# Kernel tuning notes

Measured on AMD Instinct MI355X. Metric: run time of the kernel, lower is better.

The kernel has to match this reference:

```python
import jax, jax.numpy as jnp
import numpy as np

N_NODES = 50000
N_EDGES = 640000
HID = 128
N_LAYERS = 4
BN_EPS = 1e-5


def _bn(h, gamma, beta):
    # train-mode BatchNorm1d over node axis (biased variance, as torch uses for normalization)
    mu = h.mean(axis=0)
    var = h.var(axis=0)
    return gamma * (h - mu) * jax.lax.rsqrt(var + BN_EPS) + beta


def setup_inputs() -> dict:
    key = jax.random.key(0)
    ks = jax.random.split(key, 8)
    s = 1.0 / np.sqrt(HID)
    x = jax.random.normal(ks[0], (N_NODES, HID), dtype=jnp.float32)
    edge_index = jax.random.randint(ks[1], (2, N_EDGES), 0, N_NODES, dtype=jnp.int64)
    edge_attr = jax.random.normal(ks[2], (N_EDGES, HID), dtype=jnp.float32)
    W1 = jax.random.normal(ks[3], (N_LAYERS, HID, HID), dtype=jnp.float32) * s
    b1 = jnp.zeros((N_LAYERS, HID), jnp.float32)
    g1 = jnp.ones((N_LAYERS, HID), jnp.float32)
    be1 = jnp.zeros((N_LAYERS, HID), jnp.float32)
    W2 = jax.random.normal(ks[4], (N_LAYERS, HID, HID), dtype=jnp.float32) * s
    b2 = jnp.zeros((N_LAYERS, HID), jnp.float32)
    bn_g = jnp.ones((N_LAYERS - 1, HID), jnp.float32)
    bn_b = jnp.zeros((N_LAYERS - 1, HID), jnp.float32)
    return {"x": x, "edge_index": edge_index, "edge_attr": edge_attr,
            "W1": W1, "b1": b1, "g1": g1, "be1": be1,
            "W2": W2, "b2": b2, "bn_g": bn_g, "bn_b": bn_b}


def reference(x, edge_index, edge_attr, W1, b1, g1, be1, W2, b2, bn_g, bn_b):
    src, dst = edge_index[0], edge_index[1]
    n = x.shape[0]
    z = x
    for i in range(N_LAYERS):
        # GINEConv: message = relu(x_j + e_ij), sum-aggregate, eps=0
        msg = jax.nn.relu(z[src] + edge_attr)          # [E, H]
        agg = jax.ops.segment_sum(msg, dst, num_segments=n)  # [N, H]
        h = z + agg
        # conv MLP: Linear -> BatchNorm1d -> ReLU -> Linear
        h = h @ W1[i] + b1[i]
        h = jax.nn.relu(_bn(h, g1[i], be1[i]))
        h = h @ W2[i] + b2[i]
        # encoder activation
        z = jax.nn.relu(h)
        # inter-layer batchnorm (not after last layer)
        if i != N_LAYERS - 1:
            z = _bn(z, bn_g[i], bn_b[i])
    return z
```

## Files before the change

### kernel.cpp

```cpp
#include <hip/hip_runtime.h>
#include <hip/hip_bf16.h>

#define N_NODES 50000
#define N_EDGES 640000
#define HID 128
#define BN_EPS 1e-5f
#define BF16_MAGIC 0x3F803F80u

typedef __bf16 bf16x8 __attribute__((ext_vector_type(8)));
typedef float f32x4 __attribute__((ext_vector_type(4)));

__global__ void detect_k(const unsigned int* __restrict__ g1w,
                         const unsigned int* __restrict__ idxw,
                         int* __restrict__ flags) {
    __shared__ int anynz;
    if (threadIdx.x == 0) anynz = 0;
    __syncthreads();
    unsigned int v = idxw[2 * threadIdx.x + 1];
    if (v) atomicOr(&anynz, 1);
    __syncthreads();
    if (threadIdx.x == 0) {
        flags[0] = (g1w[0] == BF16_MAGIC) ? 1 : 0;
        flags[1] = anynz ? 0 : 1;
    }
}

__global__ void init_k(int* __restrict__ cnt, float* __restrict__ statb) {
    int i = blockIdx.x * 256 + threadIdx.x;
    if (i < N_NODES) cnt[i] = 0;
    int j = i - N_NODES;
    if (j >= 0) {
        if (j < 1792) statb[j] = 0.f;
        if (j >= 2048 && j < 2176) statb[j] = 1.f;
        if (j >= 2560 && j < 2688) statb[j] = 0.f;
    }
}

__device__ __forceinline__ float cvt_in(const void* p, int i, int bf) {
    return bf ? __bfloat162float(((const __hip_bfloat16*)p)[i])
              : ((const float*)p)[i];
}

__global__ void conv_w_k(const void* W1, const void* W2, const void* b1, const void* b2,
                         const int* __restrict__ flags, float* __restrict__ wbuf) {
    int i = blockIdx.x * 256 + threadIdx.x;
    int bf = flags[0];
    if (i < 65536)       wbuf[i] = cvt_in(W1, i, bf);
    else if (i < 131072) wbuf[i] = cvt_in(W2, i - 65536, bf);
    else if (i < 131584) wbuf[i] = cvt_in(b1, i - 131072, bf);
    else if (i < 132096) wbuf[i] = cvt_in(b2, i - 131584, bf);
}

__global__ void pack_w_k(const float* __restrict__ wf,
                         __hip_bfloat16* __restrict__ hi,
                         __hip_bfloat16* __restrict__ lo) {
    int gid = blockIdx.x * 256 + threadIdx.x;
    int mat = gid >> 11;
    int ent = gid & 2047;
    int T = ent >> 8, S = (ent >> 6) & 3, L = ent & 63;
    int n = T * 16 + (L & 15);
    int k0 = S * 32 + (L >> 4) * 8;
    const float* w = wf + mat * 16384;
    __hip_bfloat16 hv[8], lv[8];
#pragma unroll
    for (int j = 0; j < 8; j++) {
        float v = w[(k0 + j) * 128 + n];
        float h = __bfloat162float(__float2bfloat16(v));
        hv[j] = __float2bfloat16(v);
        lv[j] = __float2bfloat16(v - h);
    }
    __hip_bfloat16* hp = hi + (size_t)gid * 8;
    __hip_bfloat16* lp = lo + (size_t)gid * 8;
#pragma unroll
    for (int j = 0; j < 8; j++) { hp[j] = hv[j]; lp[j] = lv[j]; }
}

__global__ void conv_x_k(const void* x, const int* __restrict__ flags,
                         float* __restrict__ zbuf) {
    int i = blockIdx.x * 256 + threadIdx.x;
    if (i < N_NODES * HID) zbuf[i] = cvt_in(x, i, flags[0]);
}

__global__ void hist_k(const void* eidx, const int* __restrict__ flags,
                       int* __restrict__ cnt) {
    int e = blockIdx.x * 256 + threadIdx.x;
    if (e >= N_EDGES) return;
    int d = flags[1] ? (int)((const long long*)eidx)[N_EDGES + e]
                     : ((const int*)eidx)[N_EDGES + e];
    atomicAdd(&cnt[d], 1);
}

__global__ void scan_k(const int* __restrict__ cnt, int* __restrict__ start,
                       int* __restrict__ cursor) {
    __shared__ int sh[1024];
    __shared__ int carry;
    if (threadIdx.x == 0) carry = 0;
    __syncthreads();
    const int CH = 8192;
    for (int base = 0; base < N_NODES; base += CH) {
        int idx0 = base + threadIdx.x * 8;
        int v[8];
        int s = 0;
#pragma unroll
        for (int j = 0; j < 8; j++) {
            int i = idx0 + j;
            v[j] = (i < N_NODES) ? cnt[i] : 0;
            s += v[j];
        }
        sh[threadIdx.x] = s;
        __syncthreads();
        for (int off = 1; off < 1024; off <<= 1) {
            int tv = 0;
            if ((int)threadIdx.x >= off) tv = sh[threadIdx.x - off];
            __syncthreads();
            if ((int)threadIdx.x >= off) sh[threadIdx.x] += tv;
            __syncthreads();
        }
        int run = sh[threadIdx.x] - s + carry;
#pragma unroll
        for (int j = 0; j < 8; j++) {
            int i = idx0 + j;
            if (i < N_NODES) { start[i] = run; cursor[i] = run; }
            run += v[j];
        }
        __syncthreads();
        if (threadIdx.x == 1023) carry += sh[1023];
        __syncthreads();
    }
    if (threadIdx.x == 0) start[N_NODES] = carry;
}

__global__ void scatter_k(const void* eidx, const int* __restrict__ flags,
                          int* __restrict__ cursor, int* __restrict__ srcs,
                          int* __restrict__ eids) {
    int e = blockIdx.x * 256 + threadIdx.x;
    if (e >= N_EDGES) return;
    int s, d;
    if (flags[1]) {
        const long long* p = (const long long*)eidx;
        s = (int)p[e]; d = (int)p[N_EDGES + e];
    } else {
        const int* p = (const int*)eidx;
        s = p[e]; d = p[N_EDGES + e];
    }
    int pos = atomicAdd(&cursor[d], 1);
    srcs[pos] = s;
    eids[pos] = e;
}

__global__ __launch_bounds__(256) void agg_k(
    const float* __restrict__ z, const void* __restrict__ eattr,
    const int* __restrict__ flags,
    const float* __restrict__ Ac, const float* __restrict__ Cc,
    const int* __restrict__ start, const int* __restrict__ srcs,
    const int* __restrict__ eids, float* __restrict__ hin) {
    int lane = threadIdx.x & 63;
    int node = blockIdx.x * 4 + (threadIdx.x >> 6);
    if (node >= N_NODES) return;
    int c0 = lane * 2;
    float ax = Ac[c0], ay = Ac[c0 + 1];
    float cx = Cc[c0], cy = Cc[c0 + 1];
    int e0 = start[node], e1 = start[node + 1];
    float sx = 0.f, sy = 0.f;
    const float2* zf = (const float2*)z;
    if (flags[0]) {
        const __hip_bfloat162* ea = (const __hip_bfloat162*)eattr;
        for (int e = e0; e < e1; e++) {
            int s = srcs[e], id = eids[e];
            float2 zv = zf[s * 64 + lane];
            float2 ev = __bfloat1622float2(ea[id * 64 + lane]);
            sx += fmaxf(fmaf(ax, zv.x, cx) + ev.x, 0.f);
            sy += fmaxf(fmaf(ay, zv.y, cy) + ev.y, 0.f);
        }
    } else {
        const float2* ea = (const float2*)eattr;
        for (int e = e0; e < e1; e++) {
            int s = srcs[e], id = eids[e];
            float2 zv = zf[s * 64 + lane];
            float2 ev = ea[id * 64 + lane];
            sx += fmaxf(fmaf(ax, zv.x, cx) + ev.x, 0.f);
            sy += fmaxf(fmaf(ay, zv.y, cy) + ev.y, 0.f);
        }
    }
    float2 zs = zf[node * 64 + lane];
    float2 o;
    o.x = fmaf(ax, zs.x, cx) + sx;
    o.y = fmaf(ay, zs.y, cy) + sy;
    ((float2*)hin)[node * 64 + lane] = o;
}

__global__ __launch_bounds__(256) void mgemm_k(
    const float* __restrict__ Ain,
    const __hip_bfloat16* __restrict__ whi, const __hip_bfloat16* __restrict__ wlo,
    const float* __restrict__ bias,
    const float* __restrict__ Ascale, const float* __restrict__ Cshift,
    float* __restrict__ Fout, void* __restrict__ OutFinal,
    const int* __restrict__ flags,
    float* __restrict__ gsum, float* __restrict__ gsq, int mode) {
    __shared__ char WshRaw[32768];
    __shared__ char WslRaw[32768];
    __shared__ float ssum[128], ssq[128];
    int t = threadIdx.x;
    int lane = t & 63, w = t >> 6, quad = lane >> 4;
    int isbf = flags[0];
    int m0 = blockIdx.x * 64;
    int row = m0 + w * 16 + (lane & 15);
    bool rv = row < N_NODES;

    bf16x8 ahi[4], alo[4];
#pragma unroll
    for (int S = 0; S < 4; S++) {
        float v[8];
        if (rv) {
            const float4* ap = (const float4*)(Ain + row * 128 + S * 32 + quad * 8);
            float4 p0 = ap[0], p1 = ap[1];
            v[0] = p0.x; v[1] = p0.y; v[2] = p0.z; v[3] = p0.w;
            v[4] = p1.x; v[5] = p1.y; v[6] = p1.z; v[7] = p1.w;
        } else {
#pragma unroll
            for (int j = 0; j < 8; j++) v[j] = 0.f;
        }
        if (mode != 0) {
            const float4* as = (const float4*)(Ascale + S * 32 + quad * 8);
            const float4* cs = (const float4*)(Cshift + S * 32 + quad * 8);
            float4 a0 = as[0], a1 = as[1], c0 = cs[0], c1 = cs[1];
            float aa[8] = {a0.x, a0.y, a0.z, a0.w, a1.x, a1.y, a1.z, a1.w};
            float cc[8] = {c0.x, c0.y, c0.z, c0.w, c1.x, c1.y, c1.z, c1.w};
#pragma unroll
            for (int j = 0; j < 8; j++) v[j] = fmaxf(fmaf(aa[j], v[j], cc[j]), 0.f);
        }
#pragma unroll
        for (int j = 0; j < 8; j++) {
            __bf16 h = (__bf16)v[j];
            ahi[S][j] = h;
            alo[S][j] = (__bf16)(v[j] - (float)h);
        }
    }

    {
        const uint4* sh = (const uint4*)whi;
        uint4* dh = (uint4*)WshRaw;
#pragma unroll
        for (int i = 0; i < 8; i++) dh[t + i * 256] = sh[t + i * 256];
        if (!isbf) {
            const uint4* sl = (const uint4*)wlo;
            uint4* dl = (uint4*)WslRaw;
#pragma unroll
            for (int i = 0; i < 8; i++) dl[t + i * 256] = sl[t + i * 256];
        }
    }
    if (t < 128) { ssum[t] = 0.f; ssq[t] = 0.f; }
    __syncthreads();

    const bf16x8* WH = (const bf16x8*)WshRaw;
    const bf16x8* WL = (const bf16x8*)WslRaw;
    f32x4 acc[8];
    f32x4 z4 = {0.f, 0.f, 0.f, 0.f};
#pragma unroll
    for (int T = 0; T < 8; T++) acc[T] = z4;
#pragma unroll
    for (int T = 0; T < 8; T++) {
#pragma unroll
        for (int S = 0; S < 4; S++) {
            bf16x8 wh = WH[(T * 4 + S) * 64 + lane];
            acc[T] = __builtin_amdgcn_mfma_f32_16x16x32_bf16(ahi[S], wh, acc[T], 0, 0, 0);
            acc[T] = __builtin_amdgcn_mfma_f32_16x16x32_bf16(alo[S], wh, acc[T], 0, 0, 0);
        }
    }
    if (!isbf) {
#pragma unroll
        for (int T = 0; T < 8; T++) {
#pragma unroll
            for (int S = 0; S < 4; S++) {
                bf16x8 wl = WL[(T * 4 + S) * 64 + lane];
                acc[T] = __builtin_amdgcn_mfma_f32_16x16x32_bf16(ahi[S], wl, acc[T], 0, 0, 0);
            }
        }
    }

    int colbase = lane & 15;
    int rbase = m0 + w * 16 + quad * 4;
#pragma unroll
    for (int T = 0; T < 8; T++) {
        int col = T * 16 + colbase;
        float bv = bias[col];
        float s = 0.f, q = 0.f;
#pragma unroll
        for (int r = 0; r < 4; r++) {
            int rr = rbase + r;
            if (rr >= N_NODES) continue;
            float o = acc[T][r] + bv;
            if (mode != 0) o = fmaxf(o, 0.f);
            if (mode == 2) {
                if (isbf) ((__hip_bfloat16*)OutFinal)[rr * 128 + col] = __float2bfloat16(o);
                else      ((float*)OutFinal)[rr * 128 + col] = o;
            } else {
                Fout[rr * 128 + col] = o;
                s += o; q += o * o;
            }
        }
        if (mode != 2) {
            s += __shfl_xor(s, 16); s += __shfl_xor(s, 32);
            q += __shfl_xor(q, 16); q += __shfl_xor(q, 32);
            if (lane < 16) { atomicAdd(&ssum[col], s); atomicAdd(&ssq[col], q); }
        }
    }
    if (mode != 2) {
        __syncthreads();
        if (t < 128) { atomicAdd(&gsum[t], ssum[t]); atomicAdd(&gsq[t], ssq[t]); }
    }
}

__global__ void fin_k(const float* __restrict__ gsum, const float* __restrict__ gsq,
                      const void* gamma, const void* beta, int layer,
                      const int* __restrict__ flags,
                      float* __restrict__ Ac, float* __restrict__ Cc) {
    int t = threadIdx.x;
    int bf = flags[0];
    float g = cvt_in(gamma, layer * 128 + t, bf);
    float b = cvt_in(beta, layer * 128 + t, bf);
    const float invN = 1.f / (float)N_NODES;
    float mean = gsum[t] * invN;
    float var = gsq[t] * invN - mean * mean;
    var = fmaxf(var, 0.f);
    float rs = rsqrtf(var + BN_EPS);
    float a = g * rs;
    Ac[t] = a;
    Cc[t] = b - mean * a;
}

extern "C" void kernel_launch(void* const* d_in, const int* in_sizes, int n_in,
                              void* d_out, int out_size, void* d_ws, size_t ws_size,
                              hipStream_t stream) {
    const void* x_p   = d_in[0];
    const void* ei_p  = d_in[1];
    const void* ea_p  = d_in[2];
    const void* W1_p  = d_in[3];
    const void* b1_p  = d_in[4];
    const void* g1_p  = d_in[5];
    const void* be1_p = d_in[6];
    const void* W2_p  = d_in[7];
    const void* b2_p  = d_in[8];
    const void* bng_p = d_in[9];
    const void* bnb_p = d_in[10];

    char* ws = (char*)d_ws;
    size_t off = 0;
    auto alloc = [&](size_t bytes) {
        void* p = ws + off;
        off += (bytes + 255) / 256 * 256;
        return p;
    };
    float* zbuf  = (float*)alloc((size_t)N_NODES * HID * 4);
    float* hin   = (float*)alloc((size_t)N_NODES * HID * 4);
    float* h1    = (float*)alloc((size_t)N_NODES * HID * 4);
    int* cnt     = (int*)alloc((size_t)N_NODES * 4);
    int* start   = (int*)alloc((size_t)(N_NODES + 1) * 4);
    int* cursor  = (int*)alloc((size_t)N_NODES * 4);
    int* srcs    = (int*)alloc((size_t)N_EDGES * 4);
    int* eids    = (int*)alloc((size_t)N_EDGES * 4);
    int* flags   = (int*)alloc(256);
    float* statb = (float*)alloc(3072 * 4);
    float* wbuf  = (float*)alloc(132096 * 4);
    __hip_bfloat16* whi_pack = (__hip_bfloat16*)alloc(8 * 16384 * 2);
    __hip_bfloat16* wlo_pack = (__hip_bfloat16*)alloc(8 * 16384 * 2);

    float* gs1  = statb;
    float* gq1  = statb + 512;
    float* gs2  = statb + 1024;
    float* gq2  = statb + 1408;
    float* A1   = statb + 1792;
    float* C1   = statb + 1920;
    float* Aagg = statb + 2048;
    float* Cagg = statb + 2560;
    float* b1f  = wbuf + 131072;
    float* b2f  = wbuf + 131584;

    detect_k<<<1, 256, 0, stream>>>((const unsigned int*)g1_p,
                                    (const unsigned int*)ei_p, flags);
    init_k<<<206, 256, 0, stream>>>(cnt, statb);
    conv_w_k<<<516, 256, 0, stream>>>(W1_p, W2_p, b1_p, b2_p, flags, wbuf);
    pack_w_k<<<64, 256, 0, stream>>>(wbuf, whi_pack, wlo_pack);
    conv_x_k<<<25000, 256, 0, stream>>>(x_p, flags, zbuf);
    hist_k<<<2500, 256, 0, stream>>>(ei_p, flags, cnt);
    scan_k<<<1, 1024, 0, stream>>>(cnt, start, cursor);
    scatter_k<<<2500, 256, 0, stream>>>(ei_p, flags, cursor, srcs, eids);

    for (int i = 0; i < 4; i++) {
        agg_k<<<12500, 256, 0, stream>>>(zbuf, ea_p, flags, Aagg + i * 128,
                                         Cagg + i * 128, start, srcs, eids, hin);
        mgemm_k<<<782, 256, 0, stream>>>(hin, whi_pack + i * 16384,
                                         wlo_pack + i * 16384, b1f + i * 128,
                                         nullptr, nullptr, h1, nullptr, flags,
                                         gs1 + i * 128, gq1 + i * 128, 0);
        fin_k<<<1, 128, 0, stream>>>(gs1 + i * 128, gq1 + i * 128, g1_p, be1_p,
                                     i, flags, A1, C1);
        if (i < 3) {
            mgemm_k<<<782, 256, 0, stream>>>(h1, whi_pack + (4 + i) * 16384,
                                             wlo_pack + (4 + i) * 16384,
                                             b2f + i * 128, A1, C1, zbuf, nullptr,
                                             flags, gs2 + i * 128, gq2 + i * 128, 1);
            fin_k<<<1, 128, 0, stream>>>(gs2 + i * 128, gq2 + i * 128, bng_p,
                                         bnb_p, i, flags, Aagg + (i + 1) * 128,
                                         Cagg + (i + 1) * 128);
        } else {
            mgemm_k<<<782, 256, 0, stream>>>(h1, whi_pack + (4 + i) * 16384,
                                             wlo_pack + (4 + i) * 16384,
                                             b2f + i * 128, A1, C1, nullptr, d_out,
                                             flags, nullptr, nullptr, 2);
        }
    }
    (void)in_sizes; (void)n_in; (void)out_size; (void)ws_size;
}
```

Before: 1.379 ms.

## Batch edge index loads via readlane, pack src/eid pairs, replace stat atomics with partials

```diff
diff --git a/kernel.cpp b/kernel.cpp
--- a/kernel.cpp
+++ b/kernel.cpp
@@ -6,6 +6,7 @@
 #define HID 128
 #define BN_EPS 1e-5f
 #define BF16_MAGIC 0x3F803F80u
+#define MG_NBLK 782
 
 typedef __bf16 bf16x8 __attribute__((ext_vector_type(8)));
 typedef float f32x4 __attribute__((ext_vector_type(4)));
@@ -78,7 +79,18 @@
 __global__ void conv_x_k(const void* x, const int* __restrict__ flags,
                          float* __restrict__ zbuf) {
     int i = blockIdx.x * 256 + threadIdx.x;
-    if (i < N_NODES * HID) zbuf[i] = cvt_in(x, i, flags[0]);
+    if (i >= N_NODES * HID / 4) return;
+    float4 o;
+    if (flags[0]) {
+        ushort4 v = ((const ushort4*)x)[i];
+        union { unsigned int u; float f; } a, b, c, d;
+        a.u = (unsigned int)v.x << 16; b.u = (unsigned int)v.y << 16;
+        c.u = (unsigned int)v.z << 16; d.u = (unsigned int)v.w << 16;
+        o.x = a.f; o.y = b.f; o.z = c.f; o.w = d.f;
+    } else {
+        o = ((const float4*)x)[i];
+    }
+    ((float4*)zbuf)[i] = o;
 }
 
 __global__ void hist_k(const void* eidx, const int* __restrict__ flags,
@@ -131,8 +143,7 @@
 }
 
 __global__ void scatter_k(const void* eidx, const int* __restrict__ flags,
-                          int* __restrict__ cursor, int* __restrict__ srcs,
-                          int* __restrict__ eids) {
+                          int* __restrict__ cursor, int2* __restrict__ se) {
     int e = blockIdx.x * 256 + threadIdx.x;
     if (e >= N_EDGES) return;
     int s, d;
@@ -144,16 +155,15 @@
         s = p[e]; d = p[N_EDGES + e];
     }
     int pos = atomicAdd(&cursor[d], 1);
-    srcs[pos] = s;
-    eids[pos] = e;
+    se[pos] = make_int2(s, e);
 }
 
 __global__ __launch_bounds__(256) void agg_k(
     const float* __restrict__ z, const void* __restrict__ eattr,
     const int* __restrict__ flags,
     const float* __restrict__ Ac, const float* __restrict__ Cc,
-    const int* __restrict__ start, const int* __restrict__ srcs,
-    const int* __restrict__ eids, float* __restrict__ hin) {
+    const int* __restrict__ start, const int2* __restrict__ se,
+    float* __restrict__ hin) {
     int lane = threadIdx.x & 63;
     int node = blockIdx.x * 4 + (threadIdx.x >> 6);
     if (node >= N_NODES) return;
@@ -161,25 +171,88 @@
     float ax = Ac[c0], ay = Ac[c0 + 1];
     float cx = Cc[c0], cy = Cc[c0 + 1];
     int e0 = start[node], e1 = start[node + 1];
+    int nE = e1 - e0;
     float sx = 0.f, sy = 0.f;
     const float2* zf = (const float2*)z;
-    if (flags[0]) {
-        const __hip_bfloat162* ea = (const __hip_bfloat162*)eattr;
-        for (int e = e0; e < e1; e++) {
-            int s = srcs[e], id = eids[e];
-            float2 zv = zf[s * 64 + lane];
-            float2 ev = __bfloat1622float2(ea[id * 64 + lane]);
-            sx += fmaxf(fmaf(ax, zv.x, cx) + ev.x, 0.f);
-            sy += fmaxf(fmaf(ay, zv.y, cy) + ev.y, 0.f);
-        }
-    } else {
-        const float2* ea = (const float2*)eattr;
-        for (int e = e0; e < e1; e++) {
-            int s = srcs[e], id = eids[e];
-            float2 zv = zf[s * 64 + lane];
-            float2 ev = ea[id * 64 + lane];
-            sx += fmaxf(fmaf(ax, zv.x, cx) + ev.x, 0.f);
-            sy += fmaxf(fmaf(ay, zv.y, cy) + ev.y, 0.f);
+    int isbf = flags[0];
+
+    for (int base = 0; base < nE; base += 64) {
+        int idx = base + lane;
+        int2 sev = se[e0 + (idx < nE ? idx : nE - 1)];
+        int rem = nE - base; if (rem > 64) rem = 64;
+        int j = 0;
+        if (isbf) {
+            const __hip_bfloat162* ea = (const __hip_bfloat162*)eattr;
+            for (; j + 4 <= rem; j += 4) {
+                int s0 = __builtin_amdgcn_readlane(sev.x, j + 0);
+                int i0 = __builtin_amdgcn_readlane(sev.y, j + 0);
+                int s1 = __builtin_amdgcn_readlane(sev.x, j + 1);
+                int i1 = __builtin_amdgcn_readlane(sev.y, j + 1);
+                int s2 = __builtin_amdgcn_readlane(sev.x, j + 2);
+                int i2 = __builtin_amdgcn_readlane(sev.y, j + 2);
+                int s3 = __builtin_amdgcn_readlane(sev.x, j + 3);
+                int i3 = __builtin_amdgcn_readlane(sev.y, j + 3);
+                float2 z0 = zf[s0 * 64 + lane];
+                float2 z1 = zf[s1 * 64 + lane];
+                float2 z2 = zf[s2 * 64 + lane];
+                float2 z3 = zf[s3 * 64 + lane];
+                float2 e0v = __bfloat1622float2(ea[i0 * 64 + lane]);
+                float2 e1v = __bfloat1622float2(ea[i1 * 64 + lane]);
+                float2 e2v = __bfloat1622float2(ea[i2 * 64 + lane]);
+                float2 e3v = __bfloat1622float2(ea[i3 * 64 + lane]);
+                sx += fmaxf(fmaf(ax, z0.x, cx) + e0v.x, 0.f);
+                sy += fmaxf(fmaf(ay, z0.y, cy) + e0v.y, 0.f);
+                sx += fmaxf(fmaf(ax, z1.x, cx) + e1v.x, 0.f);
+                sy += fmaxf(fmaf(ay, z1.y, cy) + e1v.y, 0.f);
+                sx += fmaxf(fmaf(ax, z2.x, cx) + e2v.x, 0.f);
+                sy += fmaxf(fmaf(ay, z2.y, cy) + e2v.y, 0.f);
+                sx += fmaxf(fmaf(ax, z3.x, cx) + e3v.x, 0.f);
+                sy += fmaxf(fmaf(ay, z3.y, cy) + e3v.y, 0.f);
+            }
+            for (; j < rem; j++) {
+                int s0 = __builtin_amdgcn_readlane(sev.x, j);
+                int i0 = __builtin_amdgcn_readlane(sev.y, j);
+                float2 zv = zf[s0 * 64 + lane];
+                float2 ev = __bfloat1622float2(ea[i0 * 64 + lane]);
+                sx += fmaxf(fmaf(ax, zv.x, cx) + ev.x, 0.f);
+                sy += fmaxf(fmaf(ay, zv.y, cy) + ev.y, 0.f);
+            }
+        } else {
+            const float2* ea = (const float2*)eattr;
+            for (; j + 4 <= rem; j += 4) {
+                int s0 = __builtin_amdgcn_readlane(sev.x, j + 0);
+                int i0 = __builtin_amdgcn_readlane(sev.y, j + 0);
+                int s1 = __builtin_amdgcn_readlane(sev.x, j + 1);
+                int i1 = __builtin_amdgcn_readlane(sev.y, j + 1);
+                int s2 = __builtin_amdgcn_readlane(sev.x, j + 2);
+                int i2 = __builtin_amdgcn_readlane(sev.y, j + 2);
+                int s3 = __builtin_amdgcn_readlane(sev.x, j + 3);
+                int i3 = __builtin_amdgcn_readlane(sev.y, j + 3);
+                float2 z0 = zf[s0 * 64 + lane];
+                float2 z1 = zf[s1 * 64 + lane];
+                float2 z2 = zf[s2 * 64 + lane];
+                float2 z3 = zf[s3 * 64 + lane];
+                float2 e0v = ea[i0 * 64 + lane];
+                float2 e1v = ea[i1 * 64 + lane];
+                float2 e2v = ea[i2 * 64 + lane];
+                float2 e3v = ea[i3 * 64 + lane];
+                sx += fmaxf(fmaf(ax, z0.x, cx) + e0v.x, 0.f);
+                sy += fmaxf(fmaf(ay, z0.y, cy) + e0v.y, 0.f);
+                sx += fmaxf(fmaf(ax, z1.x, cx) + e1v.x, 0.f);
+                sy += fmaxf(fmaf(ay, z1.y, cy) + e1v.y, 0.f);
+                sx += fmaxf(fmaf(ax, z2.x, cx) + e2v.x, 0.f);
+                sy += fmaxf(fmaf(ay, z2.y, cy) + e2v.y, 0.f);
+                sx += fmaxf(fmaf(ax, z3.x, cx) + e3v.x, 0.f);
+                sy += fmaxf(fmaf(ay, z3.y, cy) + e3v.y, 0.f);
+            }
+            for (; j < rem; j++) {
+                int s0 = __builtin_amdgcn_readlane(sev.x, j);
+                int i0 = __builtin_amdgcn_readlane(sev.y, j);
+                float2 zv = zf[s0 * 64 + lane];
+                float2 ev = ea[i0 * 64 + lane];
+                sx += fmaxf(fmaf(ax, zv.x, cx) + ev.x, 0.f);
+                sy += fmaxf(fmaf(ay, zv.y, cy) + ev.y, 0.f);
+            }
         }
     }
     float2 zs = zf[node * 64 + lane];
@@ -196,7 +269,7 @@
     const float* __restrict__ Ascale, const float* __restrict__ Cshift,
     float* __restrict__ Fout, void* __restrict__ OutFinal,
     const int* __restrict__ flags,
-    float* __restrict__ gsum, float* __restrict__ gsq, int mode) {
+    float* __restrict__ pbuf, int mode) {
     __shared__ char WshRaw[32768];
     __shared__ char WslRaw[32768];
     __shared__ float ssum[128], ssq[128];
@@ -307,26 +380,46 @@
     }
     if (mode != 2) {
         __syncthreads();
-        if (t < 128) { atomicAdd(&gsum[t], ssum[t]); atomicAdd(&gsq[t], ssq[t]); }
-    }
-}
-
-__global__ void fin_k(const float* __restrict__ gsum, const float* __restrict__ gsq,
+        if (t < 128) {
+            pbuf[blockIdx.x * 256 + t] = ssum[t];
+            pbuf[blockIdx.x * 256 + 128 + t] = ssq[t];
+        }
+    }
+}
+
+__global__ __launch_bounds__(256) void fin_k(const float* __restrict__ pbuf,
                       const void* gamma, const void* beta, int layer,
                       const int* __restrict__ flags,
                       float* __restrict__ Ac, float* __restrict__ Cc) {
+    int col = blockIdx.x;
     int t = threadIdx.x;
-    int bf = flags[0];
-    float g = cvt_in(gamma, layer * 128 + t, bf);
-    float b = cvt_in(beta, layer * 128 + t, bf);
-    const float invN = 1.f / (float)N_NODES;
-    float mean = gsum[t] * invN;
-    float var = gsq[t] * invN - mean * mean;
-    var = fmaxf(var, 0.f);
-    float rs = rsqrtf(var + BN_EPS);
-    float a = g * rs;
-    Ac[t] = a;
-    Cc[t] = b - mean * a;
+    float s = 0.f, q = 0.f;
+    for (int b = t; b < MG_NBLK; b += 256) {
+        s += pbuf[b * 256 + col];
+        q += pbuf[b * 256 + 128 + col];
+    }
+#pragma unroll
+    for (int m = 32; m >= 1; m >>= 1) {
+        s += __shfl_xor(s, m);
+        q += __shfl_xor(q, m);
+    }
+    __shared__ float shs[4], shq[4];
+    if ((t & 63) == 0) { shs[t >> 6] = s; shq[t >> 6] = q; }
+    __syncthreads();
+    if (t == 0) {
+        float S = shs[0] + shs[1] + shs[2] + shs[3];
+        float Q = shq[0] + shq[1] + shq[2] + shq[3];
+        int bf = flags[0];
+        float g = cvt_in(gamma, layer * 128 + col, bf);
+        float b_ = cvt_in(beta, layer * 128 + col, bf);
+        const float invN = 1.f / (float)N_NODES;
+        float mean = S * invN;
+        float var = fmaxf(Q * invN - mean * mean, 0.f);
+        float rs = rsqrtf(var + BN_EPS);
+        float a = g * rs;
+        Ac[col] = a;
+        Cc[col] = b_ - mean * a;
+    }
 }
 
 extern "C" void kernel_launch(void* const* d_in, const int* in_sizes, int n_in,
@@ -357,18 +450,14 @@
     int* cnt     = (int*)alloc((size_t)N_NODES * 4);
     int* start   = (int*)alloc((size_t)(N_NODES + 1) * 4);
     int* cursor  = (int*)alloc((size_t)N_NODES * 4);
-    int* srcs    = (int*)alloc((size_t)N_EDGES * 4);
-    int* eids    = (int*)alloc((size_t)N_EDGES * 4);
+    int2* sebuf  = (int2*)alloc((size_t)N_EDGES * 8);
     int* flags   = (int*)alloc(256);
     float* statb = (float*)alloc(3072 * 4);
     float* wbuf  = (float*)alloc(132096 * 4);
     __hip_bfloat16* whi_pack = (__hip_bfloat16*)alloc(8 * 16384 * 2);
     __hip_bfloat16* wlo_pack = (__hip_bfloat16*)alloc(8 * 16384 * 2);
-
-    float* gs1  = statb;
-    float* gq1  = statb + 512;
-    float* gs2  = statb + 1024;
-    float* gq2  = statb + 1408;
+    float* pbuf  = (float*)alloc((size_t)MG_NBLK * 256 * 4);
+
     float* A1   = statb + 1792;
     float* C1   = statb + 1920;
     float* Aagg = statb + 2048;
@@ -381,33 +470,32 @@
     init_k<<<206, 256, 0, stream>>>(cnt, statb);
     conv_w_k<<<516, 256, 0, stream>>>(W1_p, W2_p, b1_p, b2_p, flags, wbuf);
     pack_w_k<<<64, 256, 0, stream>>>(wbuf, whi_pack, wlo_pack);
-    conv_x_k<<<25000, 256, 0, stream>>>(x_p, flags, zbuf);
+    conv_x_k<<<6250, 256, 0, stream>>>(x_p, flags, zbuf);
     hist_k<<<2500, 256, 0, stream>>>(ei_p, flags, cnt);
     scan_k<<<1, 1024, 0, stream>>>(cnt, start, cursor);
-    scatter_k<<<2500, 256, 0, stream>>>(ei_p, flags, cursor, srcs, eids);
+    scatter_k<<<2500, 256, 0, stream>>>(ei_p, flags, cursor, sebuf);
 
     for (int i = 0; i < 4; i++) {
         agg_k<<<12500, 256, 0, stream>>>(zbuf, ea_p, flags, Aagg + i * 128,
-                                         Cagg + i * 128, start, srcs, eids, hin);
-        mgemm_k<<<782, 256, 0, stream>>>(hin, whi_pack + i * 16384,
+                                         Cagg + i * 128, start, sebuf, hin);
+        mgemm_k<<<MG_NBLK, 256, 0, stream>>>(hin, whi_pack + i * 16384,
                                          wlo_pack + i * 16384, b1f + i * 128,
                                          nullptr, nullptr, h1, nullptr, flags,
-                                         gs1 + i * 128, gq1 + i * 128, 0);
-        fin_k<<<1, 128, 0, stream>>>(gs1 + i * 128, gq1 + i * 128, g1_p, be1_p,
-                                     i, flags, A1, C1);
+                                         pbuf, 0);
+        fin_k<<<128, 256, 0, stream>>>(pbuf, g1_p, be1_p, i, flags, A1, C1);
         if (i < 3) {
-            mgemm_k<<<782, 256, 0, stream>>>(h1, whi_pack + (4 + i) * 16384,
+            mgemm_k<<<MG_NBLK, 256, 0, stream>>>(h1, whi_pack + (4 + i) * 16384,
                                              wlo_pack + (4 + i) * 16384,
                                              b2f + i * 128, A1, C1, zbuf, nullptr,
-                                             flags, gs2 + i * 128, gq2 + i * 128, 1);
-            fin_k<<<1, 128, 0, stream>>>(gs2 + i * 128, gq2 + i * 128, bng_p,
-                                         bnb_p, i, flags, Aagg + (i + 1) * 128,
-                                         Cagg + (i + 1) * 128);
+                                             flags, pbuf, 1);
+            fin_k<<<128, 256, 0, stream>>>(pbuf, bng_p, bnb_p, i, flags,
+                                           Aagg + (i + 1) * 128,
+                                           Cagg + (i + 1) * 128);
         } else {
-            mgemm_k<<<782, 256, 0, stream>>>(h1, whi_pack + (4 + i) * 16384,
+            mgemm_k<<<MG_NBLK, 256, 0, stream>>>(h1, whi_pack + (4 + i) * 16384,
                                              wlo_pack + (4 + i) * 16384,
                                              b2f + i * 128, A1, C1, nullptr, d_out,
-                                             flags, nullptr, nullptr, 2);
+                                             flags, pbuf, 2);
         }
     }
     (void)in_sizes; (void)n_in; (void)out_size; (void)ws_size;
```

Measured after the change: 1.185 ms. 1.16x faster.
